# Kernel tuning notes

Hardware: AMD Instinct MI355X
Metric: run time of the kernel (lower is better)

Reference implementation:

```python
import jax, jax.numpy as jnp
import numpy as np
from jax.scipy.special import gammaln, logsumexp

S, K, O, H = 64, 16, 32, 30   # state_dim, act_dim, obs_dim, horizon
T, N = 200, 512               # seq len, batch
EPS = 1e-6
LOG2PI = float(np.log(2.0 * np.pi))
NUM_PARAMS = S * O * 2 + K * S * S + S + S + 1


def setup_inputs() -> dict:
    key = jax.random.key(0)
    k1, k2, k3 = jax.random.split(key, 3)
    o = jax.random.normal(k1, (T, N, O), dtype=jnp.float32)
    a = jax.random.randint(k2, (T, N), 0, K)
    theta = jax.random.normal(k3, (N, NUM_PARAMS), dtype=jnp.float32)
    return {"o": o, "a": a, "theta": theta}


def _transform_params(theta):
    sizes = [S * O * 2, K * S * S, S, S, 1]
    idx = np.cumsum(sizes)[:-1]
    tA, tB, tC, tD, ttau = jnp.split(theta, idx, axis=-1)
    A_mean, A_lv = jnp.split(tA, 2, axis=-1)
    A_mean = A_mean.reshape(-1, S, O)
    A_std = jax.nn.softplus(A_lv.reshape(-1, S, O)) + EPS  # rectify
    B = jax.nn.softmax(tB.reshape(-1, K, S, S), axis=-1)
    C = jax.nn.softmax(tC.reshape(-1, 1, S), axis=-1)
    D = jax.nn.softmax(tD.reshape(-1, S), axis=-1)
    tau = jax.nn.sigmoid(ttau) * (2.0 * H) + 1.0  # [N,1]
    return A_mean, A_std, B, C, D, tau


def reference(o, a, theta):
    A_mean, A_std, B, C, D, tau = _transform_params(theta)

    # --- negative expected free energy reward: r[n,k,i] ---
    ent = jnp.sum(0.5 + 0.5 * LOG2PI + jnp.log(A_std), axis=-1)          # Normal entropy, [N,S]
    kl = jnp.sum(B * (jnp.log(B + EPS) - jnp.log(C[:, None] + EPS)), -1)  # KL(B || C), [N,K,S]
    eh = jnp.einsum('nkij,nj->nki', B, ent)
    r = -kl - eh

    # --- finite-horizon value iteration: q [H,N,K,S] ---
    def vi_step(qt, _):
        v = logsumexp(qt, axis=-2)                    # [N,S]
        qn = r + jnp.einsum('nkij,nj->nki', B, v)
        return qn, qn
    _, q_rest = jax.lax.scan(vi_step, r, None, length=H - 1)
    q = jnp.concatenate([r[None], q_rest], axis=0)

    # --- truncated poisson horizon weights: pdf [N,H] ---
    hh = jnp.arange(H, dtype=jnp.float32)
    logp_h = hh[None, :] * jnp.log(tau) - tau - gammaln(hh + 1.0)[None, :]
    pdf = jnp.exp(logp_h)
    pdf = pdf / jnp.sum(pdf, axis=-1, keepdims=True)

    batch_idx = jnp.arange(N)

    def time_step(b, inp):
        o_t, a_t = inp
        # policy from current belief
        qb = jnp.einsum('ni,hnki->hnk', b, q)
        pi_h = jax.nn.softmax(qb, axis=-1)
        pi_t = jnp.einsum('hnk,nh->nk', pi_h, pdf)
        # belief update
        B_a = B[batch_idx, a_t]                       # [N,S,S]
        s = jnp.einsum('nij,ni->nj', B_a, b)
        logp_s = jnp.log(s + EPS)
        lp = -0.5 * ((o_t[:, None, :] - A_mean) / A_std) ** 2 \
             - jnp.log(A_std) - 0.5 * LOG2PI          # [N,S,O]
        joint = logp_s + jnp.sum(lp, axis=-1)         # [N,S]
        b_next = jax.nn.softmax(joint, axis=-1)
        logp_o = logsumexp(joint, axis=-1)
        return b_next, (pi_t, b, logp_o)

    _, (pi, b_seq, logp_o) = jax.lax.scan(time_step, D, (o, a))
    return pi, b_seq, logp_o
```

## Files before the change

kernel.cpp:

```cpp
#include <hip/hip_runtime.h>
#include <hip/hip_bf16.h>
#include <math.h>

#define SDIM 64
#define KDIM 16
#define ODIM 32
#define HDIM 30
#define TDIM 200
#define NDIM 512
#define NP 69761
#define EPSV 1e-6f
#define LOG2PIF 1.8378770664093453f

__device__ __forceinline__ float softplusf(float x) {
    return (x > 0.f) ? x + log1pf(expf(-x)) : log1pf(expf(x));
}
__device__ __forceinline__ float wave_max64(float v) {
#pragma unroll
    for (int off = 32; off; off >>= 1) v = fmaxf(v, __shfl_xor(v, off, 64));
    return v;
}
__device__ __forceinline__ float wave_sum64(float v) {
#pragma unroll
    for (int off = 32; off; off >>= 1) v += __shfl_xor(v, off, 64);
    return v;
}
__device__ __forceinline__ void bar_lds() {
    asm volatile("s_waitcnt lgkmcnt(0)\n\ts_barrier" ::: "memory");
}

__global__ __launch_bounds__(256) void transform_kernel(
    const float* __restrict__ theta, float* __restrict__ invstd,
    float* __restrict__ c0, float* __restrict__ ent,
    float* __restrict__ logC, float* __restrict__ Dws,
    float* __restrict__ pdfws)
{
    __shared__ float ls[SDIM * 33];
    const int n = blockIdx.x, tid = threadIdx.x;
    const float* thn = theta + (size_t)n * NP;

    for (int idx = tid; idx < SDIM * ODIM; idx += 256) {
        float x = thn[2048 + idx];
        float sp = softplusf(x) + EPSV;
        invstd[(size_t)n * SDIM * ODIM + idx] = 1.f / sp;
        int s = idx >> 5, oo = idx & 31;
        ls[s * 33 + oo] = logf(sp);
    }
    __syncthreads();

    const int wave = tid >> 6, lane = tid & 63;
    if (wave == 0) {
        float sum = 0.f;
#pragma unroll
        for (int oo = 0; oo < ODIM; ++oo) sum += ls[lane * 33 + oo];
        c0[n * SDIM + lane]  = -sum - 16.f * LOG2PIF;
        ent[n * SDIM + lane] =  sum + 32.f * (0.5f + 0.5f * LOG2PIF);
    } else if (wave == 1) {
        float x = thn[69632 + lane];
        float m = wave_max64(x);
        float e = expf(x - m);
        float ssum = wave_sum64(e);
        logC[n * SDIM + lane] = logf(e / ssum + EPSV);
    } else if (wave == 2) {
        float x = thn[69696 + lane];
        float m = wave_max64(x);
        float e = expf(x - m);
        float ssum = wave_sum64(e);
        Dws[n * SDIM + lane] = e / ssum;
    } else {
        float tt = thn[69760];
        float tau = 60.f / (1.f + expf(-tt)) + 1.f;
        float p = 0.f;
        if (lane < HDIM)
            p = expf((float)lane * logf(tau) - tau - lgammaf((float)lane + 1.f));
        float ssum = wave_sum64(p);
        if (lane < HDIM) pdfws[n * HDIM + lane] = p / ssum;
    }
}

__global__ __launch_bounds__(256) void row_stats_kernel(
    const float* __restrict__ theta, const float* __restrict__ logC,
    const float* __restrict__ ent, float* __restrict__ lse,
    float* __restrict__ rws, __hip_bfloat16* __restrict__ bn)
{
    const int lane = threadIdx.x & 63;
    const int base_row = (blockIdx.x * 4 + (threadIdx.x >> 6)) * 16;
    const int n = base_row >> 10;
    const float lC = logC[n * SDIM + lane];
    const float en = ent[n * SDIM + lane];
    const float* thb = theta + (size_t)n * NP + 4096;
    unsigned short* bns = bn ? (unsigned short*)bn + (size_t)n * KDIM * SDIM * SDIM : nullptr;

#pragma unroll 1
    for (int r = 0; r < 16; ++r) {
        const int row = base_row + r;
        const int rl = row & 1023;
        float x = thb[(size_t)rl * 64 + lane];
        float m = wave_max64(x);
        float e = expf(x - m);
        float ssum = wave_sum64(e);
        float Bj = e / ssum;
        if (bns) {
            const int k = rl >> 6, i = rl & 63;
            __hip_bfloat16 h = __float2bfloat16(Bj);
            unsigned short bits;
            __builtin_memcpy(&bits, &h, 2);
            bns[(size_t)k * 4096 + (size_t)(i >> 1) * 128 + lane * 2 + (i & 1)] = bits;
        }
        float contrib = Bj * (logf(Bj + EPSV) - lC + en);
        contrib = wave_sum64(contrib);
        if (lane == 0) {
            lse[row] = m + logf(ssum);
            rws[row] = -contrib;
        }
    }
}

__global__ __launch_bounds__(512) void vi_kernel(
    const float* __restrict__ theta, const float* __restrict__ lse,
    const float* __restrict__ rws, float* __restrict__ q_ws)
{
    __shared__ float q_lds[KDIM * 68];
    __shared__ __align__(16) float v_lds[68];
    const int n = blockIdx.x, tid = threadIdx.x;
    const float* Xn = theta + (size_t)n * NP + 4096;

    const float l0  = lse[(size_t)n * 1024 + tid];
    const float l1  = lse[(size_t)n * 1024 + 512 + tid];
    const float rr0 = rws[(size_t)n * 1024 + tid];
    const float rr1 = rws[(size_t)n * 1024 + 512 + tid];

    float4 er0[16], er1[16];
    {
        const float* X0 = Xn + (size_t)tid * 64;
        const float* X1 = Xn + (size_t)(512 + tid) * 64;
#pragma unroll
        for (int j = 0; j < 16; ++j) {
            float4 x = *(const float4*)(X0 + j * 4);
            er0[j] = make_float4(__expf(x.x - l0), __expf(x.y - l0),
                                 __expf(x.z - l0), __expf(x.w - l0));
            float4 y = *(const float4*)(X1 + j * 4);
            er1[j] = make_float4(__expf(y.x - l1), __expf(y.y - l1),
                                 __expf(y.z - l1), __expf(y.w - l1));
        }
    }

    float qr0 = rr0, qr1 = rr1;
    float* qw = q_ws + (size_t)n * HDIM * 1024;
    const int kq0 = tid >> 6, iq = tid & 63;
    qw[tid] = qr0;
    qw[512 + tid] = qr1;
    q_lds[kq0 * 68 + iq] = qr0;
    q_lds[(8 + kq0) * 68 + iq] = qr1;
    __syncthreads();

#pragma unroll 1
    for (int h = 1; h < HDIM; ++h) {
        if (tid < 64) {
            float m = -1e30f;
#pragma unroll
            for (int k = 0; k < KDIM; ++k) m = fmaxf(m, q_lds[k * 68 + tid]);
            float s = 0.f;
#pragma unroll
            for (int k = 0; k < KDIM; ++k) s += __expf(q_lds[k * 68 + tid] - m);
            v_lds[tid] = m + __logf(s);
        }
        bar_lds();
        float a0x = 0.f, a0y = 0.f, a0z = 0.f, a0w = 0.f;
        float a1x = 0.f, a1y = 0.f, a1z = 0.f, a1w = 0.f;
#pragma unroll
        for (int jq = 0; jq < 16; ++jq) {
            const float4 v4 = *(const float4*)&v_lds[jq * 4];
            a0x += er0[jq].x * v4.x; a0y += er0[jq].y * v4.y;
            a0z += er0[jq].z * v4.z; a0w += er0[jq].w * v4.w;
            a1x += er1[jq].x * v4.x; a1y += er1[jq].y * v4.y;
            a1z += er1[jq].z * v4.z; a1w += er1[jq].w * v4.w;
        }
        qr0 = rr0 + ((a0x + a0y) + (a0z + a0w));
        qr1 = rr1 + ((a1x + a1y) + (a1z + a1w));
        qw[(size_t)h * 1024 + tid] = qr0;
        qw[(size_t)h * 1024 + 512 + tid] = qr1;
        q_lds[kq0 * 68 + iq] = qr0;
        q_lds[(8 + kq0) * 68 + iq] = qr1;
        bar_lds();
    }
}

#define BSP(T_, U_) do {                                                       \
    const int cur_ = (T_) & 1, nxt_ = cur_ ^ 1;                                \
    if (wave == 3) out_b[((size_t)(T_) * NDIM + n) * SDIM + lane] = bval;      \
    if (wave == 1) b2_s[cur_][lane] = bval;                                    \
    {                                       \
        float a0_ = 0.f, a1_ = 0.f, a2_ = 0.f, a3_ = 0.f;                      \
        _Pragma("unroll")                                                      \
        for (int j_ = 0; j_ < 4; ++j_) {                                       \
            a0_ += er[4 * j_ + 0] * __shfl(bval, rbase + 4 * j_ + 0, 64);      \
            a1_ += er[4 * j_ + 1] * __shfl(bval, rbase + 4 * j_ + 1, 64);      \
            a2_ += er[4 * j_ + 2] * __shfl(bval, rbase + 4 * j_ + 2, 64);      \
            a3_ += er[4 * j_ + 3] * __shfl(bval, rbase + 4 * j_ + 3, 64);      \
        }                                                                      \
        part_s[cur_][wave][lane] = (a0_ + a1_) + (a2_ + a3_);                  \
    }                                                                          \
    if ((T_) + 1 < TDIM) {                             \
        const float* om_ = &o_s[((T_) + 1) * ODIM + ob];                       \
        float zz_ = 0.f;                                                       \
        _Pragma("unroll")                                                      \
        for (int j_ = 0; j_ < 8; ++j_) {                                       \
            float z_ = (om_[j_] - mean_r[j_]) * istd_r[j_];                    \
            zz_ += z_ * z_;                                                    \
        }                                                                      \
        z2p_s[nxt_][wave][lane] = zz_;                                         \
    }                                                                          \
    _Pragma("unroll")                             \
    for (int m_ = 0; m_ < 8; ++m_) {                                           \
        er[2 * m_]     = __uint_as_float(U_[m_] << 16);                        \
        er[2 * m_ + 1] = __uint_as_float(U_[m_] & 0xffff0000u);                \
    }                                                                          \
    {                                                 \
        const int tl_ = ((T_) + 3 < TDIM) ? (T_) + 3 : TDIM - 1;               \
        const uint* up_ = bnn32 + (size_t)a_s[tl_] * 2048 + (rbase >> 1) * 64 + lane; \
        _Pragma("unroll")                                                      \
        for (int m_ = 0; m_ < 8; ++m_) U_[m_] = up_[m_ * 64];                  \
    }                                                                          \
    bar_lds();                                            \
    {                   \
        float sv_ = part_s[cur_][0][lane] + part_s[cur_][1][lane]              \
                  + part_s[cur_][2][lane] + part_s[cur_][3][lane];             \
        float u_ = (sv_ + EPSV) * ecz_cur;                                     \
        float S_ = wave_sum64(u_);                                             \
        if (wave == 0 && lane == 0)                                            \
            out_lp[(size_t)(T_) * NDIM + n] = cm_cur + __logf(S_);             \
        bval = u_ / S_;                                                        \
        float z2n_ = z2p_s[nxt_][0][lane] + z2p_s[nxt_][1][lane]               \
                   + z2p_s[nxt_][2][lane] + z2p_s[nxt_][3][lane];              \
        float cn_ = c0_r - 0.5f * z2n_;                                        \
        cm_cur = wave_max64(cn_);                                              \
        ecz_cur = __expf(cn_ - cm_cur);                                        \
    }                                                                          \
    {                     \
        float aAx_ = 0.f, aAy_ = 0.f, aAz_ = 0.f, aAw_ = 0.f;                  \
        float aBx_ = 0.f, aBy_ = 0.f, aBz_ = 0.f, aBw_ = 0.f;                  \
        _Pragma("unroll")                                                      \
        for (int jq_ = 0; jq_ < 16; ++jq_) {                                   \
            const float4 b4_ = *(const float4*)&b2_s[cur_][jq_ * 4];           \
            aAx_ += qA[jq_].x * b4_.x; aAy_ += qA[jq_].y * b4_.y;              \
            aAz_ += qA[jq_].z * b4_.z; aAw_ += qA[jq_].w * b4_.w;              \
            aBx_ += qB[jq_].x * b4_.x; aBy_ += qB[jq_].y * b4_.y;              \
            aBz_ += qB[jq_].z * b4_.z; aBw_ += qB[jq_].w * b4_.w;              \
        }                                                                      \
        float aA_ = (aAx_ + aAy_) + (aAz_ + aAw_);                             \
        float aB_ = (aBx_ + aBy_) + (aBz_ + aBw_);                             \
        float mA_ = aA_, mB_ = aB_;                                            \
        mA_ = fmaxf(mA_, __shfl_xor(mA_, 1, 64));                              \
        mB_ = fmaxf(mB_, __shfl_xor(mB_, 1, 64));                              \
        mA_ = fmaxf(mA_, __shfl_xor(mA_, 2, 64));                              \
        mB_ = fmaxf(mB_, __shfl_xor(mB_, 2, 64));                              \
        mA_ = fmaxf(mA_, __shfl_xor(mA_, 4, 64));                              \
        mB_ = fmaxf(mB_, __shfl_xor(mB_, 4, 64));                              \
        mA_ = fmaxf(mA_, __shfl_xor(mA_, 8, 64));                              \
        mB_ = fmaxf(mB_, __shfl_xor(mB_, 8, 64));                              \
        float eA_ = __expf(aA_ - mA_), eB_ = __expf(aB_ - mB_);                \
        float SA_ = eA_, SB_ = eB_;                                            \
        SA_ += __shfl_xor(SA_, 1, 64);  SB_ += __shfl_xor(SB_, 1, 64);         \
        SA_ += __shfl_xor(SA_, 2, 64);  SB_ += __shfl_xor(SB_, 2, 64);         \
        SA_ += __shfl_xor(SA_, 4, 64);  SB_ += __shfl_xor(SB_, 4, 64);         \
        SA_ += __shfl_xor(SA_, 8, 64);  SB_ += __shfl_xor(SB_, 8, 64);         \
        float val_ = pdfA * eA_ / SA_ + pdfB * eB_ / SB_;                      \
        val_ += __shfl_xor(val_, 16, 64);                                      \
        val_ += __shfl_xor(val_, 32, 64);                                      \
        if (lane < 16) p2_s[cur_][wave][lane] = val_;                          \
        if ((T_) > 0 && wave == 3 && lane < 16) {                              \
            float s4_ = p2_s[nxt_][0][lane] + p2_s[nxt_][1][lane]              \
                      + p2_s[nxt_][2][lane] + p2_s[nxt_][3][lane];             \
            out_pi[((size_t)((T_) - 1) * NDIM + n) * KDIM + lane] = s4_;       \
        }                                                                      \
    }                                                                          \
} while (0)

__global__ __launch_bounds__(256, 2) void bp_kernel(
    const float* __restrict__ o, const int* __restrict__ a,
    const float* __restrict__ theta, const __hip_bfloat16* __restrict__ bn,
    const float* __restrict__ invstd, const float* __restrict__ c0g,
    const float* __restrict__ Dws, const float* __restrict__ pdfg,
    const float* __restrict__ q_ws,
    float* __restrict__ out_pi, float* __restrict__ out_b,
    float* __restrict__ out_lp)
{
    __shared__ float o_s[TDIM * ODIM];
    __shared__ int   a_s[TDIM];
    __shared__ float mean_s[SDIM * 33];
    __shared__ float istd_s[SDIM * 33];
    __shared__ float c0_sh[SDIM];
    __shared__ float part_s[2][4][68];
    __shared__ float z2p_s[2][4][SDIM];
    __shared__ __align__(16) float b2_s[2][SDIM];
    __shared__ float p2_s[2][4][17];

    const int n = blockIdx.x, tid = threadIdx.x;
    const int wave = tid >> 6, lane = tid & 63;
    const int rbase = wave * 16, ob = wave * 8;
    const float* thn = theta + (size_t)n * NP;
    const uint* bnn32 = (const uint*)(bn + (size_t)n * KDIM * SDIM * SDIM);

    for (int idx = tid; idx < TDIM * ODIM; idx += 256)
        o_s[idx] = o[((size_t)(idx >> 5) * NDIM + n) * ODIM + (idx & 31)];
    if (tid < TDIM) a_s[tid] = a[tid * NDIM + n];
    for (int idx = tid; idx < SDIM * ODIM; idx += 256) {
        int s = idx >> 5, oo = idx & 31;
        mean_s[s * 33 + oo] = thn[idx];
        istd_s[s * 33 + oo] = invstd[(size_t)n * SDIM * ODIM + idx];
    }
    if (tid < SDIM) c0_sh[tid] = c0g[n * SDIM + tid];

    const int hA = tid >> 4, kA = tid & 15, hB = hA + 16;
    const float* qnp = q_ws + (size_t)n * HDIM * 1024;
    float4 qA[16], qB[16];
#pragma unroll
    for (int jq = 0; jq < 16; ++jq)
        qA[jq] = *(const float4*)&qnp[(size_t)hA * 1024 + kA * 64 + jq * 4];
    if (hB < HDIM) {
#pragma unroll
        for (int jq = 0; jq < 16; ++jq)
            qB[jq] = *(const float4*)&qnp[(size_t)hB * 1024 + kA * 64 + jq * 4];
    } else {
#pragma unroll
        for (int jq = 0; jq < 16; ++jq) qB[jq] = make_float4(0.f, 0.f, 0.f, 0.f);
    }
    const float pdfA = pdfg[n * HDIM + hA];
    const float pdfB = (hB < HDIM) ? pdfg[n * HDIM + hB] : 0.f;
    __syncthreads();

    const float c0_r = c0_sh[lane];
    float bval = Dws[n * SDIM + lane];
    float mean_r[8], istd_r[8];
#pragma unroll
    for (int j = 0; j < 8; ++j) {
        mean_r[j] = mean_s[lane * 33 + ob + j];
        istd_r[j] = istd_s[lane * 33 + ob + j];
    }

    float er[16];
    uint u0[8], u1[8];
    {
        const uint* p0 = bnn32 + (size_t)a_s[0] * 2048 + (rbase >> 1) * 64 + lane;
#pragma unroll
        for (int m = 0; m < 8; ++m) u0[m] = p0[m * 64];
#pragma unroll
        for (int m = 0; m < 8; ++m) {
            er[2 * m]     = __uint_as_float(u0[m] << 16);
            er[2 * m + 1] = __uint_as_float(u0[m] & 0xffff0000u);
        }
        const uint* p1 = bnn32 + (size_t)a_s[1] * 2048 + (rbase >> 1) * 64 + lane;
#pragma unroll
        for (int m = 0; m < 8; ++m) u0[m] = p1[m * 64];
        const uint* p2 = bnn32 + (size_t)a_s[2] * 2048 + (rbase >> 1) * 64 + lane;
#pragma unroll
        for (int m = 0; m < 8; ++m) u1[m] = p2[m * 64];
    }
    {
        const float* om = &o_s[ob];
        float zz = 0.f;
#pragma unroll
        for (int j = 0; j < 8; ++j) {
            float z = (om[j] - mean_r[j]) * istd_r[j];
            zz += z * z;
        }
        z2p_s[0][wave][lane] = zz;
    }
    __syncthreads();
    float ecz_cur, cm_cur;
    {
        float z2 = z2p_s[0][0][lane] + z2p_s[0][1][lane]
                 + z2p_s[0][2][lane] + z2p_s[0][3][lane];
        float c = c0_r - 0.5f * z2;
        cm_cur = wave_max64(c);
        ecz_cur = __expf(c - cm_cur);
    }

#pragma unroll 1
    for (int t = 0; t < TDIM; t += 2) {
        BSP(t, u0);
        BSP(t + 1, u1);
    }
    __syncthreads();
    if (wave == 3 && lane < 16) {
        float s4 = p2_s[1][0][lane] + p2_s[1][1][lane]
                 + p2_s[1][2][lane] + p2_s[1][3][lane];
        out_pi[((size_t)(TDIM - 1) * NDIM + n) * KDIM + lane] = s4;
    }
}

#define Z2PART(TT_, BUF_) do {                                                 \
    const int ob_ = (wave - 1) * 8;                                            \
    const float* om_ = &o_s[(TT_) * ODIM + ob_];                               \
    float zz_ = 0.f;                                                           \
    _Pragma("unroll")                                                          \
    for (int j_ = 0; j_ < 8; ++j_) {                                           \
        float z_ = (om_[j_] - mean_s[lane * 33 + ob_ + j_])                    \
                 * istd_s[lane * 33 + ob_ + j_];                               \
        zz_ += z_ * z_;                                                        \
    }                                                                          \
    z2p_s[BUF_][wave - 1][lane] = zz_;                                         \
} while (0)

#define BSTEP(T_, RAW_) do {                                                   \
    const int cur_ = (T_) & 1, nxt_ = cur_ ^ 1;                                \
    if (wave >= 1) {                                                           \
        float acc_ = 0.f;                                                      \
        _Pragma("unroll")                                                      \
        for (int ii = 0; ii < 10; ++ii)                                        \
            if (ii < nrow) acc_ += er[ii] * b_s[cur_][rbase + ii];             \
        part_s[wave - 1][lane] = acc_;                                         \
        if (wave == 6) out_b[((size_t)(T_) * NDIM + n) * SDIM + lane] = b_s[cur_][lane]; \
    }                                                                          \
    bar_lds();                                                                 \
    if (wave == 0) {                                                           \
        float sv_ = part_s[0][lane] + part_s[1][lane] + part_s[2][lane]        \
                  + part_s[3][lane] + part_s[4][lane] + part_s[5][lane]        \
                  + part_s[6][lane];                                           \
        float z2_ = z2p_s[cur_][0][lane] + z2p_s[cur_][1][lane]                \
                  + z2p_s[cur_][2][lane] + z2p_s[cur_][3][lane];               \
        float joint_ = __logf(sv_ + EPSV) + c0_s[lane] - 0.5f * z2_;           \
        float m_ = wave_max64(joint_);                                         \
        float e_ = __expf(joint_ - m_);                                        \
        float ss_ = wave_sum64(e_);                                            \
        b_s[nxt_][lane] = e_ / ss_;                                            \
        if (lane == 0) out_lp[(size_t)(T_) * NDIM + n] = m_ + __logf(ss_);     \
    } else {                                                                   \
        if ((T_) + 1 < TDIM) {                                                 \
            const int an_ = a_s[(T_) + 1];                                     \
            const float* ln_ = lseA + an_ * SDIM;                              \
            _Pragma("unroll")                                                  \
            for (int ii = 0; ii < 10; ++ii)                                    \
                if (ii < nrow) er[ii] = __expf(RAW_[ii] - ln_[rbase + ii]);    \
            if (wave <= 4) Z2PART((T_) + 1, nxt_);                             \
        }                                                                      \
        const int tl_ = ((T_) + 3 < TDIM) ? (T_) + 3 : TDIM - 1;               \
        const int a3_ = a_s[tl_];                                              \
        const float* X3_ = Xn + (size_t)a3_ * SDIM * SDIM;                     \
        _Pragma("unroll")                                                      \
        for (int ii = 0; ii < 10; ++ii)                                        \
            if (ii < nrow) RAW_[ii] = X3_[(size_t)(rbase + ii) * SDIM + lane]; \
    }                                                                          \
    bar_lds();                                                                 \
} while (0)

__global__ __launch_bounds__(512) void belief_kernel(
    const float* __restrict__ o, const int* __restrict__ a,
    const float* __restrict__ theta, const float* __restrict__ lse,
    const float* __restrict__ invstd, const float* __restrict__ c0g,
    const float* __restrict__ Dws,
    float* __restrict__ out_b, float* __restrict__ out_lp)
{
    __shared__ float o_s[TDIM * ODIM];
    __shared__ int   a_s[TDIM];
    __shared__ float mean_s[SDIM * 33];
    __shared__ float istd_s[SDIM * 33];
    __shared__ float lseA[KDIM * SDIM];
    __shared__ float c0_s[SDIM];
    __shared__ float b_s[2][SDIM];
    __shared__ float part_s[7][68];
    __shared__ float z2p_s[2][4][SDIM];

    const int n = blockIdx.x, tid = threadIdx.x;
    const int wave = tid >> 6, lane = tid & 63;
    const float* thn = theta + (size_t)n * NP;
    const float* Xn  = thn + 4096;

    for (int idx = tid; idx < TDIM * ODIM; idx += 512)
        o_s[idx] = o[((size_t)(idx >> 5) * NDIM + n) * ODIM + (idx & 31)];
    if (tid < TDIM) a_s[tid] = a[tid * NDIM + n];
    for (int idx = tid; idx < SDIM * ODIM; idx += 512) {
        int s = idx >> 5, oo = idx & 31;
        mean_s[s * 33 + oo] = thn[idx];
        istd_s[s * 33 + oo] = invstd[(size_t)n * SDIM * ODIM + idx];
    }
    for (int idx = tid; idx < KDIM * SDIM; idx += 512)
        lseA[idx] = lse[(size_t)n * KDIM * SDIM + idx];
    if (tid < SDIM) { c0_s[tid] = c0g[n * SDIM + tid]; b_s[0][tid] = Dws[n * SDIM + tid]; }
    __syncthreads();

    const int rbase = (wave >= 1) ? (wave - 1) * 10 : 0;
    const int nrow  = (wave >= 1) ? ((SDIM - rbase) < 10 ? (SDIM - rbase) : 10) : 0;

    float er[10], raw0[10], raw1[10];
    if (wave >= 1) {
        const int a0 = a_s[0];
        const float* X0 = Xn + (size_t)a0 * SDIM * SDIM;
        const float* l0 = lseA + a0 * SDIM;
#pragma unroll
        for (int ii = 0; ii < 10; ++ii)
            if (ii < nrow) er[ii] = __expf(X0[(size_t)(rbase + ii) * SDIM + lane] - l0[rbase + ii]);
        const int a1 = a_s[1];
        const float* X1 = Xn + (size_t)a1 * SDIM * SDIM;
#pragma unroll
        for (int ii = 0; ii < 10; ++ii)
            if (ii < nrow) raw0[ii] = X1[(size_t)(rbase + ii) * SDIM + lane];
        const int a2 = a_s[2];
        const float* X2 = Xn + (size_t)a2 * SDIM * SDIM;
#pragma unroll
        for (int ii = 0; ii < 10; ++ii)
            if (ii < nrow) raw1[ii] = X2[(size_t)(rbase + ii) * SDIM + lane];
        if (wave <= 4) Z2PART(0, 0);
    }
    __syncthreads();

#pragma unroll 1
    for (int t = 0; t < TDIM; t += 2) {
        BSTEP(t, raw0);
        BSTEP(t + 1, raw1);
    }
}

__global__ __launch_bounds__(512) void vi_policy_kernel(
    const float* __restrict__ theta, const float* __restrict__ lse,
    const float* __restrict__ rws, const float* __restrict__ pdfg,
    const float* __restrict__ out_b_g, float* __restrict__ out_pi)
{
    __shared__ __align__(16) float q_s[HDIM * KDIM * 68];
    __shared__ float r_s[KDIM * SDIM];
    __shared__ float lse_s[KDIM * SDIM];
    __shared__ __align__(16) float v_s[SDIM];
    __shared__ __align__(16) float b_lds[64 * 68];
    __shared__ float pdf_s[32];

    const int n = blockIdx.x, tid = threadIdx.x;
    const int wave = tid >> 6, lane = tid & 63;
    const int sub = lane & 15, rq = lane >> 4;
    const float* Xn = theta + (size_t)n * NP + 4096;

    for (int idx = tid; idx < KDIM * SDIM; idx += 512) {
        r_s[idx]   = rws[(size_t)n * KDIM * SDIM + idx];
        lse_s[idx] = lse[(size_t)n * KDIM * SDIM + idx];
    }
    if (tid < HDIM) pdf_s[tid] = pdfg[n * HDIM + tid];
    __syncthreads();

    for (int idx = tid; idx < KDIM * SDIM; idx += 512)
        q_s[(idx >> 6) * 68 + (idx & 63)] = r_s[idx];

    float4 breg[32];
#pragma unroll
    for (int it = 0; it < 32; ++it) {
        const int row = it * 32 + wave * 4 + rq;
        const float* xr = Xn + (size_t)row * SDIM + sub * 4;
        const float l = lse_s[row];
        breg[it] = make_float4(__expf(xr[0] - l), __expf(xr[1] - l),
                               __expf(xr[2] - l), __expf(xr[3] - l));
    }
    bar_lds();

#pragma unroll 1
    for (int h = 1; h < HDIM; ++h) {
        if (tid < SDIM) {
            const int base = (h - 1) * KDIM;
            float m = -1e30f;
#pragma unroll
            for (int k = 0; k < KDIM; ++k) m = fmaxf(m, q_s[(base + k) * 68 + tid]);
            float ssum = 0.f;
#pragma unroll
            for (int k = 0; k < KDIM; ++k) ssum += __expf(q_s[(base + k) * 68 + tid] - m);
            v_s[tid] = m + __logf(ssum);
        }
        bar_lds();
        const float4 v4 = *(const float4*)&v_s[sub * 4];
#pragma unroll
        for (int it = 0; it < 32; ++it) {
            const int row = it * 32 + wave * 4 + rq;
            float acc = breg[it].x * v4.x + breg[it].y * v4.y
                      + breg[it].z * v4.z + breg[it].w * v4.w;
            acc += __shfl_xor(acc, 1, 64);
            acc += __shfl_xor(acc, 2, 64);
            acc += __shfl_xor(acc, 4, 64);
            acc += __shfl_xor(acc, 8, 64);
            if (sub == 0)
                q_s[(h * KDIM + (row >> 6)) * 68 + (row & 63)] = r_s[row] + acc;
        }
        bar_lds();
    }

    const int tc = tid >> 4, kk = tid & 15;
#pragma unroll 1
    for (int t0 = 0; t0 < TDIM; t0 += 64) {
        const int nt = (TDIM - t0) < 64 ? (TDIM - t0) : 64;
        for (int idx = tid; idx < nt * 16; idx += 512) {
            const int row = idx >> 4, jq = idx & 15;
            *(float4*)&b_lds[row * 68 + jq * 4] =
                *(const float4*)&out_b_g[(((size_t)(t0 + row)) * NDIM + n) * SDIM + jq * 4];
        }
        bar_lds();
        const bool vA = tc < nt, vB = (tc + 32) < nt;
        float4 bqA[16], bqB[16];
        if (vA) {
#pragma unroll
            for (int jq = 0; jq < 16; ++jq)
                bqA[jq] = *(const float4*)&b_lds[tc * 68 + jq * 4];
        }
        if (vB) {
#pragma unroll
            for (int jq = 0; jq < 16; ++jq)
                bqB[jq] = *(const float4*)&b_lds[(tc + 32) * 68 + jq * 4];
        }
        float pikA = 0.f, pikB = 0.f;
#pragma unroll 1
        for (int h = 0; h < HDIM; ++h) {
            const float* qr = &q_s[(h * KDIM + kk) * 68];
            float aA = 0.f, aB = 0.f;
#pragma unroll
            for (int jq = 0; jq < 16; ++jq) {
                const float4 qv = *(const float4*)&qr[jq * 4];
                if (vA) aA += qv.x * bqA[jq].x + qv.y * bqA[jq].y
                            + qv.z * bqA[jq].z + qv.w * bqA[jq].w;
                if (vB) aB += qv.x * bqB[jq].x + qv.y * bqB[jq].y
                            + qv.z * bqB[jq].z + qv.w * bqB[jq].w;
            }
            float mA = aA, mB = aB;
            mA = fmaxf(mA, __shfl_xor(mA, 1, 64));
            mA = fmaxf(mA, __shfl_xor(mA, 2, 64));
            mA = fmaxf(mA, __shfl_xor(mA, 4, 64));
            mA = fmaxf(mA, __shfl_xor(mA, 8, 64));
            mB = fmaxf(mB, __shfl_xor(mB, 1, 64));
            mB = fmaxf(mB, __shfl_xor(mB, 2, 64));
            mB = fmaxf(mB, __shfl_xor(mB, 4, 64));
            mB = fmaxf(mB, __shfl_xor(mB, 8, 64));
            float eA = __expf(aA - mA), eB = __expf(aB - mB);
            float SA = eA, SB = eB;
            SA += __shfl_xor(SA, 1, 64);
            SA += __shfl_xor(SA, 2, 64);
            SA += __shfl_xor(SA, 4, 64);
            SA += __shfl_xor(SA, 8, 64);
            SB += __shfl_xor(SB, 1, 64);
            SB += __shfl_xor(SB, 2, 64);
            SB += __shfl_xor(SB, 4, 64);
            SB += __shfl_xor(SB, 8, 64);
            const float ph = pdf_s[h];
            pikA += ph * eA / SA;
            pikB += ph * eB / SB;
        }
        if (vA) out_pi[(((size_t)(t0 + tc)) * NDIM + n) * KDIM + kk] = pikA;
        if (vB) out_pi[(((size_t)(t0 + 32 + tc)) * NDIM + n) * KDIM + kk] = pikB;
        bar_lds();
    }
}

extern "C" void kernel_launch(void* const* d_in, const int* in_sizes, int n_in,
                              void* d_out, int out_size, void* d_ws, size_t ws_size,
                              hipStream_t stream) {
    (void)in_sizes; (void)n_in; (void)out_size;
    const float* o     = (const float*)d_in[0];
    const int*   a     = (const int*)d_in[1];
    const float* theta = (const float*)d_in[2];
    float* out = (float*)d_out;
    float* ws  = (float*)d_ws;

    float* lse    = ws;
    float* rws    = lse    + (size_t)NDIM * KDIM * SDIM;
    float* invstd = rws    + (size_t)NDIM * KDIM * SDIM;
    float* c0     = invstd + (size_t)NDIM * SDIM * ODIM;
    float* ent    = c0     + (size_t)NDIM * SDIM;
    float* logC   = ent    + (size_t)NDIM * SDIM;
    float* Dws    = logC   + (size_t)NDIM * SDIM;
    float* pdfws  = Dws    + (size_t)NDIM * SDIM;
    float* q_ws   = pdfws  + (size_t)NDIM * HDIM;
    __hip_bfloat16* bn = (__hip_bfloat16*)(q_ws + (size_t)NDIM * HDIM * KDIM * SDIM);

    const size_t f_base = (size_t)NDIM * KDIM * SDIM * 2
                        + (size_t)NDIM * SDIM * ODIM
                        + (size_t)NDIM * SDIM * 4
                        + (size_t)NDIM * HDIM;
    const size_t f_q  = (size_t)NDIM * HDIM * KDIM * SDIM;
    const size_t need1 = (f_base + f_q) * 4
                       + (size_t)NDIM * KDIM * SDIM * SDIM * 2;

    float* out_pi = out;
    float* out_b  = out + (size_t)TDIM * NDIM * KDIM;
    float* out_lp = out + (size_t)TDIM * NDIM * KDIM + (size_t)TDIM * NDIM * SDIM;

    transform_kernel<<<NDIM, 256, 0, stream>>>(theta, invstd, c0, ent, logC, Dws, pdfws);

    if (ws_size >= need1) {
        row_stats_kernel<<<8192, 256, 0, stream>>>(theta, logC, ent, lse, rws, bn);
        vi_kernel<<<NDIM, 512, 0, stream>>>(theta, lse, rws, q_ws);
        bp_kernel<<<NDIM, 256, 0, stream>>>(
            o, a, theta, bn, invstd, c0, Dws, pdfws, q_ws, out_pi, out_b, out_lp);
    } else {
        row_stats_kernel<<<8192, 256, 0, stream>>>(
            theta, logC, ent, lse, rws, (__hip_bfloat16*)nullptr);
        belief_kernel<<<NDIM, 512, 0, stream>>>(
            o, a, theta, lse, invstd, c0, Dws, out_b, out_lp);
        vi_policy_kernel<<<NDIM, 512, 0, stream>>>(theta, lse, rws, pdfws, out_b, out_pi);
    }
}
```

Baseline: 590.1 us.

## Fuse transform, row-stats and value iteration into one prep kernel; bf16 belief in LDS

Merges the transform, row-statistics and value-iteration kernels into a single per-batch prep kernel. Intermediates (logC, ent, lse, rws) now stay in shared memory instead of going through global memory, and two kernel launches are removed. The belief-propagation kernel also stores the belief vector in LDS as packed bf16 for the q·b dot product, which halves LDS reads but lowers precision of the policy logits. The row-stats work now runs on only 512 blocks of 8 waves each, where it previously ran on 8192 blocks, so it gets less parallelism.

Measured after the change: 799.6 us. 35.5% more time.

```diff
diff --git a/kernel.cpp b/kernel.cpp
--- a/kernel.cpp
+++ b/kernel.cpp
@@ -29,17 +29,24 @@
     asm volatile("s_waitcnt lgkmcnt(0)\n\ts_barrier" ::: "memory");
 }
 
-__global__ __launch_bounds__(256) void transform_kernel(
+__global__ __launch_bounds__(512) void prep_kernel(
     const float* __restrict__ theta, float* __restrict__ invstd,
-    float* __restrict__ c0, float* __restrict__ ent,
-    float* __restrict__ logC, float* __restrict__ Dws,
-    float* __restrict__ pdfws)
+    float* __restrict__ c0, float* __restrict__ Dws,
+    float* __restrict__ pdfws, __hip_bfloat16* __restrict__ bn,
+    float* __restrict__ q_ws)
 {
     __shared__ float ls[SDIM * 33];
+    __shared__ float logC_s[SDIM], ent_s[SDIM];
+    __shared__ float lse_s[1024];
+    __shared__ float rws_s[1024];
+    __shared__ float q_lds[KDIM * 68];
+    __shared__ __align__(16) float v_lds[68];
+
     const int n = blockIdx.x, tid = threadIdx.x;
+    const int wave = tid >> 6, lane = tid & 63;
     const float* thn = theta + (size_t)n * NP;
 
-    for (int idx = tid; idx < SDIM * ODIM; idx += 256) {
+    for (int idx = tid; idx < SDIM * ODIM; idx += 512) {
         float x = thn[2048 + idx];
         float sp = softplusf(x) + EPSV;
         invstd[(size_t)n * SDIM * ODIM + idx] = 1.f / sp;
@@ -47,27 +54,25 @@
         ls[s * 33 + oo] = logf(sp);
     }
     __syncthreads();
-
-    const int wave = tid >> 6, lane = tid & 63;
     if (wave == 0) {
         float sum = 0.f;
 #pragma unroll
         for (int oo = 0; oo < ODIM; ++oo) sum += ls[lane * 33 + oo];
-        c0[n * SDIM + lane]  = -sum - 16.f * LOG2PIF;
-        ent[n * SDIM + lane] =  sum + 32.f * (0.5f + 0.5f * LOG2PIF);
+        c0[n * SDIM + lane] = -sum - 16.f * LOG2PIF;
+        ent_s[lane] = sum + 32.f * (0.5f + 0.5f * LOG2PIF);
     } else if (wave == 1) {
         float x = thn[69632 + lane];
         float m = wave_max64(x);
         float e = expf(x - m);
         float ssum = wave_sum64(e);
-        logC[n * SDIM + lane] = logf(e / ssum + EPSV);
+        logC_s[lane] = logf(e / ssum + EPSV);
     } else if (wave == 2) {
         float x = thn[69696 + lane];
         float m = wave_max64(x);
         float e = expf(x - m);
         float ssum = wave_sum64(e);
         Dws[n * SDIM + lane] = e / ssum;
-    } else {
+    } else if (wave == 3) {
         float tt = thn[69760];
         float tau = 60.f / (1.f + expf(-tt)) + 1.f;
         float p = 0.f;
@@ -76,62 +81,41 @@
         float ssum = wave_sum64(p);
         if (lane < HDIM) pdfws[n * HDIM + lane] = p / ssum;
     }
-}
-
-__global__ __launch_bounds__(256) void row_stats_kernel(
-    const float* __restrict__ theta, const float* __restrict__ logC,
-    const float* __restrict__ ent, float* __restrict__ lse,
-    float* __restrict__ rws, __hip_bfloat16* __restrict__ bn)
-{
-    const int lane = threadIdx.x & 63;
-    const int base_row = (blockIdx.x * 4 + (threadIdx.x >> 6)) * 16;
-    const int n = base_row >> 10;
-    const float lC = logC[n * SDIM + lane];
-    const float en = ent[n * SDIM + lane];
-    const float* thb = theta + (size_t)n * NP + 4096;
-    unsigned short* bns = bn ? (unsigned short*)bn + (size_t)n * KDIM * SDIM * SDIM : nullptr;
-
-#pragma unroll 1
-    for (int r = 0; r < 16; ++r) {
-        const int row = base_row + r;
-        const int rl = row & 1023;
-        float x = thb[(size_t)rl * 64 + lane];
-        float m = wave_max64(x);
-        float e = expf(x - m);
-        float ssum = wave_sum64(e);
-        float Bj = e / ssum;
-        if (bns) {
-            const int k = rl >> 6, i = rl & 63;
+    __syncthreads();
+
+    {
+        unsigned short* bns = (unsigned short*)bn + (size_t)n * KDIM * SDIM * SDIM;
+        const float lC = logC_s[lane], en = ent_s[lane];
+        const float* thb = thn + 4096;
+#pragma unroll 2
+        for (int r = 0; r < 128; ++r) {
+            const int row = wave * 128 + r;
+            float x = thb[(size_t)row * 64 + lane];
+            float m = wave_max64(x);
+            float e = expf(x - m);
+            float ssum = wave_sum64(e);
+            float Bj = e / ssum;
+            const int k = row >> 6, i = row & 63;
             __hip_bfloat16 h = __float2bfloat16(Bj);
             unsigned short bits;
             __builtin_memcpy(&bits, &h, 2);
             bns[(size_t)k * 4096 + (size_t)(i >> 1) * 128 + lane * 2 + (i & 1)] = bits;
-        }
-        float contrib = Bj * (logf(Bj + EPSV) - lC + en);
-        contrib = wave_sum64(contrib);
-        if (lane == 0) {
-            lse[row] = m + logf(ssum);
-            rws[row] = -contrib;
-        }
-    }
-}
-
-__global__ __launch_bounds__(512) void vi_kernel(
-    const float* __restrict__ theta, const float* __restrict__ lse,
-    const float* __restrict__ rws, float* __restrict__ q_ws)
-{
-    __shared__ float q_lds[KDIM * 68];
-    __shared__ __align__(16) float v_lds[68];
-    const int n = blockIdx.x, tid = threadIdx.x;
-    const float* Xn = theta + (size_t)n * NP + 4096;
-
-    const float l0  = lse[(size_t)n * 1024 + tid];
-    const float l1  = lse[(size_t)n * 1024 + 512 + tid];
-    const float rr0 = rws[(size_t)n * 1024 + tid];
-    const float rr1 = rws[(size_t)n * 1024 + 512 + tid];
-
-    float4 er0[16], er1[16];
+            float contrib = Bj * (logf(Bj + EPSV) - lC + en);
+            contrib = wave_sum64(contrib);
+            if (lane == 0) {
+                lse_s[row] = m + logf(ssum);
+                rws_s[row] = -contrib;
+            }
+        }
+    }
+    __syncthreads();
+
     {
+        const float* Xn = thn + 4096;
+        const float l0 = lse_s[tid], l1 = lse_s[512 + tid];
+        const float rr0 = rws_s[tid], rr1 = rws_s[512 + tid];
+
+        float4 er0[16], er1[16];
         const float* X0 = Xn + (size_t)tid * 64;
         const float* X1 = Xn + (size_t)(512 + tid) * 64;
 #pragma unroll
@@ -143,54 +127,65 @@
             er1[j] = make_float4(__expf(y.x - l1), __expf(y.y - l1),
                                  __expf(y.z - l1), __expf(y.w - l1));
         }
-    }
-
-    float qr0 = rr0, qr1 = rr1;
-    float* qw = q_ws + (size_t)n * HDIM * 1024;
-    const int kq0 = tid >> 6, iq = tid & 63;
-    qw[tid] = qr0;
-    qw[512 + tid] = qr1;
-    q_lds[kq0 * 68 + iq] = qr0;
-    q_lds[(8 + kq0) * 68 + iq] = qr1;
-    __syncthreads();
-
-#pragma unroll 1
-    for (int h = 1; h < HDIM; ++h) {
-        if (tid < 64) {
-            float m = -1e30f;
-#pragma unroll
-            for (int k = 0; k < KDIM; ++k) m = fmaxf(m, q_lds[k * 68 + tid]);
-            float s = 0.f;
-#pragma unroll
-            for (int k = 0; k < KDIM; ++k) s += __expf(q_lds[k * 68 + tid] - m);
-            v_lds[tid] = m + __logf(s);
-        }
-        bar_lds();
-        float a0x = 0.f, a0y = 0.f, a0z = 0.f, a0w = 0.f;
-        float a1x = 0.f, a1y = 0.f, a1z = 0.f, a1w = 0.f;
-#pragma unroll
-        for (int jq = 0; jq < 16; ++jq) {
-            const float4 v4 = *(const float4*)&v_lds[jq * 4];
-            a0x += er0[jq].x * v4.x; a0y += er0[jq].y * v4.y;
-            a0z += er0[jq].z * v4.z; a0w += er0[jq].w * v4.w;
-            a1x += er1[jq].x * v4.x; a1y += er1[jq].y * v4.y;
-            a1z += er1[jq].z * v4.z; a1w += er1[jq].w * v4.w;
-        }
-        qr0 = rr0 + ((a0x + a0y) + (a0z + a0w));
-        qr1 = rr1 + ((a1x + a1y) + (a1z + a1w));
-        qw[(size_t)h * 1024 + tid] = qr0;
-        qw[(size_t)h * 1024 + 512 + tid] = qr1;
+
+        float qr0 = rr0, qr1 = rr1;
+        float* qw = q_ws + (size_t)n * HDIM * 1024;
+        const int kq0 = tid >> 6, iq = tid & 63;
+        qw[tid] = qr0;
+        qw[512 + tid] = qr1;
         q_lds[kq0 * 68 + iq] = qr0;
         q_lds[(8 + kq0) * 68 + iq] = qr1;
-        bar_lds();
+        __syncthreads();
+
+#pragma unroll 1
+        for (int h = 1; h < HDIM; ++h) {
+            if (tid < 64) {
+                float m = -1e30f;
+#pragma unroll
+                for (int k = 0; k < KDIM; ++k) m = fmaxf(m, q_lds[k * 68 + tid]);
+                float s = 0.f;
+#pragma unroll
+                for (int k = 0; k < KDIM; ++k) s += __expf(q_lds[k * 68 + tid] - m);
+                v_lds[tid] = m + __logf(s);
+            }
+            bar_lds();
+            float a0x = 0.f, a0y = 0.f, a0z = 0.f, a0w = 0.f;
+            float a1x = 0.f, a1y = 0.f, a1z = 0.f, a1w = 0.f;
+#pragma unroll
+            for (int jq = 0; jq < 16; ++jq) {
+                const float4 v4 = *(const float4*)&v_lds[jq * 4];
+                a0x += er0[jq].x * v4.x; a0y += er0[jq].y * v4.y;
+                a0z += er0[jq].z * v4.z; a0w += er0[jq].w * v4.w;
+                a1x += er1[jq].x * v4.x; a1y += er1[jq].y * v4.y;
+                a1z += er1[jq].z * v4.z; a1w += er1[jq].w * v4.w;
+            }
+            qr0 = rr0 + ((a0x + a0y) + (a0z + a0w));
+            qr1 = rr1 + ((a1x + a1y) + (a1z + a1w));
+            qw[(size_t)h * 1024 + tid] = qr0;
+            qw[(size_t)h * 1024 + 512 + tid] = qr1;
+            q_lds[kq0 * 68 + iq] = qr0;
+            q_lds[(8 + kq0) * 68 + iq] = qr1;
+            bar_lds();
+        }
     }
 }
 
 #define BSP(T_, U_) do {                                                       \
     const int cur_ = (T_) & 1, nxt_ = cur_ ^ 1;                                \
     if (wave == 3) out_b[((size_t)(T_) * NDIM + n) * SDIM + lane] = bval;      \
-    if (wave == 1) b2_s[cur_][lane] = bval;                                    \
-    {                                       \
+    if (wave == 2) {                               \
+        float eA_ = __shfl(bval, 2 * (lane & 31), 64);                         \
+        float eB_ = __shfl(bval, 2 * (lane & 31) + 1, 64);                     \
+        if (lane < 32) {                                                       \
+            __hip_bfloat16 hA_ = __float2bfloat16(eA_);                        \
+            __hip_bfloat16 hB_ = __float2bfloat16(eB_);                        \
+            unsigned short ba_, bb_;                                           \
+            __builtin_memcpy(&ba_, &hA_, 2);                                   \
+            __builtin_memcpy(&bb_, &hB_, 2);                                   \
+            b2u_s[cur_][lane] = (uint)ba_ | ((uint)bb_ << 16);                 \
+        }                                                                      \
+    }                                                                          \
+    {                                \
         float a0_ = 0.f, a1_ = 0.f, a2_ = 0.f, a3_ = 0.f;                      \
         _Pragma("unroll")                                                      \
         for (int j_ = 0; j_ < 4; ++j_) {                                       \
@@ -237,16 +232,31 @@
         cm_cur = wave_max64(cn_);                                              \
         ecz_cur = __expf(cn_ - cm_cur);                                        \
     }                                                                          \
-    {                     \
+    {               \
+        const uint4* bp_ = (const uint4*)&b2u_s[cur_][0];                      \
         float aAx_ = 0.f, aAy_ = 0.f, aAz_ = 0.f, aAw_ = 0.f;                  \
         float aBx_ = 0.f, aBy_ = 0.f, aBz_ = 0.f, aBw_ = 0.f;                  \
         _Pragma("unroll")                                                      \
-        for (int jq_ = 0; jq_ < 16; ++jq_) {                                   \
-            const float4 b4_ = *(const float4*)&b2_s[cur_][jq_ * 4];           \
-            aAx_ += qA[jq_].x * b4_.x; aAy_ += qA[jq_].y * b4_.y;              \
-            aAz_ += qA[jq_].z * b4_.z; aAw_ += qA[jq_].w * b4_.w;              \
-            aBx_ += qB[jq_].x * b4_.x; aBy_ += qB[jq_].y * b4_.y;              \
-            aBz_ += qB[jq_].z * b4_.z; aBw_ += qB[jq_].w * b4_.w;              \
+        for (int r_ = 0; r_ < 8; ++r_) {                                       \
+            const uint4 u_ = bp_[r_];                                          \
+            const float b0_ = __uint_as_float(u_.x << 16);                     \
+            const float b1_ = __uint_as_float(u_.x & 0xffff0000u);             \
+            const float b2_ = __uint_as_float(u_.y << 16);                     \
+            const float b3_ = __uint_as_float(u_.y & 0xffff0000u);             \
+            const float b4_ = __uint_as_float(u_.z << 16);                     \
+            const float b5_ = __uint_as_float(u_.z & 0xffff0000u);             \
+            const float b6_ = __uint_as_float(u_.w << 16);                     \
+            const float b7_ = __uint_as_float(u_.w & 0xffff0000u);             \
+            const float4 qa0_ = qA[2 * r_], qb0_ = qA[2 * r_ + 1];             \
+            const float4 qa1_ = qB[2 * r_], qb1_ = qB[2 * r_ + 1];             \
+            aAx_ += qa0_.x * b0_; aAy_ += qa0_.y * b1_;                        \
+            aAz_ += qa0_.z * b2_; aAw_ += qa0_.w * b3_;                        \
+            aAx_ += qb0_.x * b4_; aAy_ += qb0_.y * b5_;                        \
+            aAz_ += qb0_.z * b6_; aAw_ += qb0_.w * b7_;                        \
+            aBx_ += qa1_.x * b0_; aBy_ += qa1_.y * b1_;                        \
+            aBz_ += qa1_.z * b2_; aBw_ += qa1_.w * b3_;                        \
+            aBx_ += qb1_.x * b4_; aBy_ += qb1_.y * b5_;                        \
+            aBz_ += qb1_.z * b6_; aBw_ += qb1_.w * b7_;                        \
         }                                                                      \
         float aA_ = (aAx_ + aAy_) + (aAz_ + aAw_);                             \
         float aB_ = (aBx_ + aBy_) + (aBz_ + aBw_);                             \
@@ -293,7 +303,7 @@
     __shared__ float c0_sh[SDIM];
     __shared__ float part_s[2][4][68];
     __shared__ float z2p_s[2][4][SDIM];
-    __shared__ __align__(16) float b2_s[2][SDIM];
+    __shared__ __align__(16) uint b2u_s[2][32];
     __shared__ float p2_s[2][4][17];
 
     const int n = blockIdx.x, tid = threadIdx.x;
@@ -387,6 +397,85 @@
         float s4 = p2_s[1][0][lane] + p2_s[1][1][lane]
                  + p2_s[1][2][lane] + p2_s[1][3][lane];
         out_pi[((size_t)(TDIM - 1) * NDIM + n) * KDIM + lane] = s4;
+    }
+}
+
+__global__ __launch_bounds__(256) void transform_kernel(
+    const float* __restrict__ theta, float* __restrict__ invstd,
+    float* __restrict__ c0, float* __restrict__ ent,
+    float* __restrict__ logC, float* __restrict__ Dws,
+    float* __restrict__ pdfws)
+{
+    __shared__ float ls[SDIM * 33];
+    const int n = blockIdx.x, tid = threadIdx.x;
+    const float* thn = theta + (size_t)n * NP;
+
+    for (int idx = tid; idx < SDIM * ODIM; idx += 256) {
+        float x = thn[2048 + idx];
+        float sp = softplusf(x) + EPSV;
+        invstd[(size_t)n * SDIM * ODIM + idx] = 1.f / sp;
+        int s = idx >> 5, oo = idx & 31;
+        ls[s * 33 + oo] = logf(sp);
+    }
+    __syncthreads();
+
+    const int wave = tid >> 6, lane = tid & 63;
+    if (wave == 0) {
+        float sum = 0.f;
+#pragma unroll
+        for (int oo = 0; oo < ODIM; ++oo) sum += ls[lane * 33 + oo];
+        c0[n * SDIM + lane]  = -sum - 16.f * LOG2PIF;
+        ent[n * SDIM + lane] =  sum + 32.f * (0.5f + 0.5f * LOG2PIF);
+    } else if (wave == 1) {
+        float x = thn[69632 + lane];
+        float m = wave_max64(x);
+        float e = expf(x - m);
+        float ssum = wave_sum64(e);
+        logC[n * SDIM + lane] = logf(e / ssum + EPSV);
+    } else if (wave == 2) {
+        float x = thn[69696 + lane];
+        float m = wave_max64(x);
+        float e = expf(x - m);
+        float ssum = wave_sum64(e);
+        Dws[n * SDIM + lane] = e / ssum;
+    } else {
+        float tt = thn[69760];
+        float tau = 60.f / (1.f + expf(-tt)) + 1.f;
+        float p = 0.f;
+        if (lane < HDIM)
+            p = expf((float)lane * logf(tau) - tau - lgammaf((float)lane + 1.f));
+        float ssum = wave_sum64(p);
+        if (lane < HDIM) pdfws[n * HDIM + lane] = p / ssum;
+    }
+}
+
+__global__ __launch_bounds__(256) void row_stats_kernel(
+    const float* __restrict__ theta, const float* __restrict__ logC,
+    const float* __restrict__ ent, float* __restrict__ lse,
+    float* __restrict__ rws)
+{
+    const int lane = threadIdx.x & 63;
+    const int base_row = (blockIdx.x * 4 + (threadIdx.x >> 6)) * 16;
+    const int n = base_row >> 10;
+    const float lC = logC[n * SDIM + lane];
+    const float en = ent[n * SDIM + lane];
+    const float* thb = theta + (size_t)n * NP + 4096;
+
+#pragma unroll 1
+    for (int r = 0; r < 16; ++r) {
+        const int row = base_row + r;
+        const int rl = row & 1023;
+        float x = thb[(size_t)rl * 64 + lane];
+        float m = wave_max64(x);
+        float e = expf(x - m);
+        float ssum = wave_sum64(e);
+        float Bj = e / ssum;
+        float contrib = Bj * (logf(Bj + EPSV) - lC + en);
+        contrib = wave_sum64(contrib);
+        if (lane == 0) {
+            lse[row] = m + logf(ssum);
+            rws[row] = -contrib;
+        }
     }
 }
 
@@ -676,16 +765,13 @@
     float* out_b  = out + (size_t)TDIM * NDIM * KDIM;
     float* out_lp = out + (size_t)TDIM * NDIM * KDIM + (size_t)TDIM * NDIM * SDIM;
 
-    transform_kernel<<<NDIM, 256, 0, stream>>>(theta, invstd, c0, ent, logC, Dws, pdfws);
-
     if (ws_size >= need1) {
-        row_stats_kernel<<<8192, 256, 0, stream>>>(theta, logC, ent, lse, rws, bn);
-        vi_kernel<<<NDIM, 512, 0, stream>>>(theta, lse, rws, q_ws);
+        prep_kernel<<<NDIM, 512, 0, stream>>>(theta, invstd, c0, Dws, pdfws, bn, q_ws);
         bp_kernel<<<NDIM, 256, 0, stream>>>(
             o, a, theta, bn, invstd, c0, Dws, pdfws, q_ws, out_pi, out_b, out_lp);
     } else {
-        row_stats_kernel<<<8192, 256, 0, stream>>>(
-            theta, logC, ent, lse, rws, (__hip_bfloat16*)nullptr);
+        transform_kernel<<<NDIM, 256, 0, stream>>>(theta, invstd, c0, ent, logC, Dws, pdfws);
+        row_stats_kernel<<<8192, 256, 0, stream>>>(theta, logC, ent, lse, rws);
         belief_kernel<<<NDIM, 512, 0, stream>>>(
             o, a, theta, lse, invstd, c0, Dws, out_b, out_lp);
         vi_policy_kernel<<<NDIM, 512, 0, stream>>>(theta, lse, rws, pdfws, out_b, out_pi);
```
